# Performance work log

Measured on AMD Instinct MI355X. Metric: run time of the kernel, lower is better.

Reference implementation:

```python
import jax, jax.numpy as jnp
import numpy as np

B, S, E, NH = 1, 2048, 1024, 8
DH = E // NH
EPS_BACKEND = 1e-6  # eps in parallel_stabilized_simple
EPS_NORM = 1e-5     # MultiHeadLayerNorm (group_norm) eps


def setup_inputs() -> dict:
    key = jax.random.key(0)
    ks = jax.random.split(key, 8)
    q = jax.random.normal(ks[0], (B, S, E), jnp.float32)
    k = jax.random.normal(ks[1], (B, S, E), jnp.float32)
    v = jax.random.normal(ks[2], (B, S, E), jnp.float32)
    # gate Linear params: weight (NH, 3E), bias (NH). Small scale so gates are
    # in a realistic regime (fgate bias ~ linspace(3,6) per the torch init).
    igate_w = jax.random.normal(ks[3], (NH, 3 * E), jnp.float32) * 0.02
    igate_b = jax.random.normal(ks[4], (NH,), jnp.float32) * 0.1
    fgate_w = jax.random.normal(ks[5], (NH, 3 * E), jnp.float32) * 0.02
    fgate_b = jnp.linspace(3.0, 6.0, NH).astype(jnp.float32)
    norm_w = 1.0 + 0.1 * jax.random.normal(ks[6], (E,), jnp.float32)
    return dict(q=q, k=k, v=v, igate_w=igate_w, igate_b=igate_b,
                fgate_w=fgate_w, fgate_b=fgate_b, norm_w=norm_w)


def reference(q, k, v, igate_w, igate_b, fgate_w, fgate_b, norm_w):
    Bq, Sq, Eq = q.shape
    nh = igate_w.shape[0]
    dh = Eq // nh
    # gate pre-activations from concatenated q,k,v
    gate_in = jnp.concatenate([q, k, v], axis=-1)             # (B,S,3E)
    ig = jnp.transpose(gate_in @ igate_w.T + igate_b, (0, 2, 1))  # (B,NH,S)
    fg = jnp.transpose(gate_in @ fgate_w.T + fgate_b, (0, 2, 1))  # (B,NH,S)
    # split heads: (B,NH,S,DH)
    qh = q.reshape(Bq, Sq, nh, dh).transpose(0, 2, 1, 3)
    kh = k.reshape(Bq, Sq, nh, dh).transpose(0, 2, 1, 3)
    vh = v.reshape(Bq, Sq, nh, dh).transpose(0, 2, 1, 3)
    # cumulative log forget gates; decay matrix entry (t,s) = cs[t]-cs[s]
    log_f_cum = jnp.cumsum(jax.nn.log_sigmoid(fg), axis=-1)   # (B,NH,S)
    log_fg_mat = log_f_cum[:, :, :, None] - log_f_cum[:, :, None, :]  # (B,NH,S,S)
    ltr = jnp.tril(jnp.ones((Sq, Sq), dtype=bool))            # causal mask
    log_D = jnp.where(ltr, log_fg_mat + ig[:, :, None, :], -jnp.inf)
    # row-wise stabilizer
    max_log_D = jnp.max(log_D, axis=-1, keepdims=True)        # (B,NH,S,1)
    D = jnp.exp(log_D - max_log_D)
    qk = jnp.einsum('bhsd,bhtd->bhst', qh, kh) / jnp.sqrt(jnp.float32(dh))
    C = qk * D
    normalizer = jnp.maximum(jnp.abs(jnp.sum(C, axis=-1, keepdims=True)),
                             jnp.exp(-max_log_D))
    h = jnp.einsum('bhst,bhtd->bhsd', C / (normalizer + EPS_BACKEND), vh)
    # MultiHeadLayerNorm == group_norm with NH groups over (NH*DH), per-channel weight
    mean = jnp.mean(h, axis=-1, keepdims=True)
    var = jnp.var(h, axis=-1, keepdims=True)
    h_norm = (h - mean) / jnp.sqrt(var + EPS_NORM)
    h_norm = h_norm * norm_w.reshape(nh, dh)[None, :, None, :]
    return h_norm.transpose(0, 2, 1, 3).reshape(Bq, Sq, Eq)
```

## Files before the change

kernel.cpp:

```cpp
#include <hip/hip_runtime.h>
#include <hip/hip_bf16.h>
#include <math.h>

#define S_LEN 2048
#define E_DIM 1024
#define NHEAD 8
#define DH 128
#define E3 3072

typedef short bf16x8 __attribute__((ext_vector_type(8)));
typedef short bf16x4 __attribute__((ext_vector_type(4)));
typedef float f32x4 __attribute__((ext_vector_type(4)));
typedef float f32x16 __attribute__((ext_vector_type(16)));

#define MFMA3216(a,b,c) __builtin_amdgcn_mfma_f32_32x32x16_bf16(a,b,c,0,0,0)
#define Z16 {0.f,0.f,0.f,0.f,0.f,0.f,0.f,0.f,0.f,0.f,0.f,0.f,0.f,0.f,0.f,0.f}
#define CROW(r) (((r)&3) + 8*((r)>>2))

__device__ __forceinline__ unsigned short f2bf(float f){
  union{float f; unsigned u;} x; x.f = f;
  unsigned r = x.u + 0x7FFF + ((x.u>>16)&1);
  return (unsigned short)(r>>16);
}

__device__ __forceinline__ unsigned cvtpk(float lo, float hi){
  unsigned r;
  asm("v_cvt_pk_bf16_f32 %0, %1, %2" : "=v"(r) : "v"(lo), "v"(hi));
  return r;
}

__device__ __forceinline__ float logsigf(float x){
  return fminf(x, 0.f) - log1pf(expf(-fabsf(x)));
}

typedef const __attribute__((address_space(1))) unsigned int* gas1_t;
typedef __attribute__((address_space(3))) unsigned int* las3_t;
__device__ __forceinline__ void stage16(const ushort* g, ushort* l){
  __builtin_amdgcn_global_load_lds((gas1_t)(const void*)g, (las3_t)(void*)l, 16, 0, 0);
}

__global__ __launch_bounds__(256) void gates_qk(
    const float* __restrict__ q, const float* __restrict__ k, const float* __restrict__ v,
    const float* __restrict__ igw, const float* __restrict__ igb,
    const float* __restrict__ fgw, const float* __restrict__ fgb,
    float* __restrict__ ig_out, float* __restrict__ lsf_out,
    ushort* __restrict__ qbo, ushort* __restrict__ kbo, ushort* __restrict__ vto){
  const int t0 = blockIdx.x*4;
  const int tid = threadIdx.x;
  const int lane = tid & 63, wv = tid >> 6;
  float acc[64];
  #pragma unroll
  for (int a=0;a<64;++a) acc[a]=0.f;
  const float sc = 0.08838834764831845f;
  #pragma unroll
  for (int step=0; step<3; ++step){
    const float* src = (step==0)? q : ((step==1)? k : v);
    float4 in4[4];
    #pragma unroll
    for (int r=0;r<4;++r) in4[r] = ((const float4*)src)[(size_t)(t0+r)*256 + tid];
    if (step==0){
      #pragma unroll
      for (int r=0;r<4;++r){
        ushort4 o; o.x=f2bf(in4[r].x*sc); o.y=f2bf(in4[r].y*sc);
        o.z=f2bf(in4[r].z*sc); o.w=f2bf(in4[r].w*sc);
        ((ushort4*)qbo)[(size_t)(t0+r)*256 + tid] = o;
      }
    } else if (step==1){
      #pragma unroll
      for (int r=0;r<4;++r){
        ushort4 o; o.x=f2bf(in4[r].x); o.y=f2bf(in4[r].y);
        o.z=f2bf(in4[r].z); o.w=f2bf(in4[r].w);
        ((ushort4*)kbo)[(size_t)(t0+r)*256 + tid] = o;
      }
    } else {
      #pragma unroll
      for (int c=0;c<4;++c){
        ushort4 ov;
        ov.x = f2bf(((const float*)&in4[0])[c]);
        ov.y = f2bf(((const float*)&in4[1])[c]);
        ov.z = f2bf(((const float*)&in4[2])[c]);
        ov.w = f2bf(((const float*)&in4[3])[c]);
        *(ushort4*)(vto + (size_t)(tid*4+c)*S_LEN + t0) = ov;
      }
    }
    const int wj = step*256 + tid;
    #pragma unroll
    for (int o=0;o<8;++o){
      float4 wI = ((const float4*)igw)[o*768 + wj];
      float4 wF = ((const float4*)fgw)[o*768 + wj];
      #pragma unroll
      for (int r=0;r<4;++r){
        acc[o*4+r]    = fmaf(in4[r].x, wI.x, acc[o*4+r]);
        acc[o*4+r]    = fmaf(in4[r].y, wI.y, acc[o*4+r]);
        acc[o*4+r]    = fmaf(in4[r].z, wI.z, acc[o*4+r]);
        acc[o*4+r]    = fmaf(in4[r].w, wI.w, acc[o*4+r]);
        acc[32+o*4+r] = fmaf(in4[r].x, wF.x, acc[32+o*4+r]);
        acc[32+o*4+r] = fmaf(in4[r].y, wF.y, acc[32+o*4+r]);
        acc[32+o*4+r] = fmaf(in4[r].z, wF.z, acc[32+o*4+r]);
        acc[32+o*4+r] = fmaf(in4[r].w, wF.w, acc[32+o*4+r]);
      }
    }
  }
  int cnt = 32;
  #pragma unroll
  for (int s=0; s<6; ++s){
    const bool hib = (lane >> s) & 1;
    #pragma unroll
    for (int a=0; a<32; ++a){
      if (a < cnt){
        float sent = hib ? acc[a] : acc[a+cnt];
        float got = __shfl_xor(sent, 1<<s, 64);
        acc[a] = (hib ? acc[a+cnt] : acc[a]) + got;
      }
    }
    cnt >>= 1;
  }
  __shared__ float red[4][64];
  red[wv][lane] = acc[0];
  __syncthreads();
  if (tid < 64){
    float tot = red[0][tid]+red[1][tid]+red[2][tid]+red[3][tid];
    int a = (int)(__brev((unsigned)tid) >> 26);
    int f = a >> 5, o = (a>>2)&7, r = a&3;
    int t = t0 + r;
    if (f==0) ig_out[o*S_LEN + t] = tot + igb[o];
    else      lsf_out[o*S_LEN + t] = logsigf(tot + fgb[o]);
  }
}

__global__ __launch_bounds__(256) void scan_kernel(
    const float* __restrict__ ig, const float* __restrict__ lsf,
    float* __restrict__ cs_out, float* __restrict__ M_out, float* __restrict__ m_out){
  const int h = blockIdx.x;
  const int tid = threadIdx.x;
  __shared__ float tt[256];
  const int base = tid*8;
  const float* src = lsf + h*S_LEN;
  float loc[8]; float tot = 0.f;
  #pragma unroll
  for (int i=0;i<8;++i){ tot += src[base+i]; loc[i]=tot; }
  tt[tid]=tot; __syncthreads();
  for (int off=1; off<256; off<<=1){
    float add = (tid>=off)? tt[tid-off] : 0.f;
    __syncthreads();
    tt[tid] += add;
    __syncthreads();
  }
  const float excl = tt[tid] - tot;
  float csv[8];
  #pragma unroll
  for (int i=0;i<8;++i){ csv[i] = excl + loc[i]; cs_out[h*S_LEN+base+i]=csv[i]; }
  const float* igp = ig + h*S_LEN;
  float mloc[8], mval[8]; float mtot = -INFINITY;
  #pragma unroll
  for (int i=0;i<8;++i){
    float m = igp[base+i] - csv[i];
    mval[i] = m;
    mtot = fmaxf(mtot, m);
    mloc[i] = mtot;
  }
  __syncthreads();
  tt[tid]=mtot; __syncthreads();
  for (int off=1; off<256; off<<=1){
    float add = (tid>=off)? tt[tid-off] : -INFINITY;
    __syncthreads();
    tt[tid] = fmaxf(tt[tid], add);
    __syncthreads();
  }
  const float exclm = (tid>0)? tt[tid-1] : -INFINITY;
  #pragma unroll
  for (int i=0;i<8;++i){
    M_out[h*S_LEN+base+i] = fmaxf(exclm, mloc[i]);
    m_out[h*S_LEN+base+i] = mval[i];
  }
}

__global__ __launch_bounds__(256, 2) void mlstm_mfma6(
    const ushort* __restrict__ qb, const ushort* __restrict__ kb,
    const ushort* __restrict__ vt,
    const float* __restrict__ csb, const float* __restrict__ Mxb,
    const float* __restrict__ mbb,
    const float* __restrict__ nw, float* __restrict__ out){
  const int h = blockIdx.x;
  const int qt = 63 - blockIdx.y;
  const int tid = threadIdx.x, l = tid & 63;
  const int sq = tid >> 6;
  const int l31 = l & 31, l15 = l & 15, hi = l >> 5;

  __shared__ __align__(16) float UNI[4*32*132];
  __shared__ float MB[128];
  __shared__ float rsL[4][32];
  ushort* Kb = (ushort*)UNI;
  ushort* Vb = Kb + 16384;
  float*  Part = UNI;

  const int hS = h*S_LEN;
  const ushort* kbh = kb + h*DH;
  const ushort* vth = vt + (size_t)h*DH*S_LEN;
  const float*  mh  = mbb + hS;
  const int t0 = qt*32;
  const int NT = (t0 + 31)/128 + 1;
  const int tgq = t0 + l31;
  const float Mq = Mxb[hS + tgq];

  bf16x8 qf0,qf1,qf2,qf3,qf4,qf5,qf6,qf7;
  { const ushort* qs = qb + (size_t)tgq*E_DIM + h*DH + hi*8;
    qf0 = *(const bf16x8*)(qs+0);   qf1 = *(const bf16x8*)(qs+16);
    qf2 = *(const bf16x8*)(qs+32);  qf3 = *(const bf16x8*)(qs+48);
    qf4 = *(const bf16x8*)(qs+64);  qf5 = *(const bf16x8*)(qs+80);
    qf6 = *(const bf16x8*)(qs+96);  qf7 = *(const bf16x8*)(qs+112); }

  f32x16 a0 = Z16, a1 = Z16, a2 = Z16, a3 = Z16;
  float rsq = 0.f;

#define STAGE6(ktv) {                                                        \
    _Pragma("unroll")                                                        \
    for (int i_=0;i_<8;++i_){                                                \
      const int L_ = tid + i_*256; const int row_ = L_>>4, pc_ = L_&15;      \
      stage16(kbh + (size_t)((ktv)*128+row_)*E_DIM + ((pc_^(row_&15))<<3),   \
              Kb + (size_t)L_*8); }                                          \
    _Pragma("unroll")                                                        \
    for (int i_=0;i_<8;++i_){                                                \
      const int L_ = tid + i_*256; const int d_ = L_>>4, pc_ = L_&15;        \
      stage16(vth + (size_t)d_*S_LEN + (ktv)*128 + ((pc_^(d_&15))<<3),       \
              Vb + (size_t)L_*8); }                                          \
    if (tid < 32)                                                            \
      stage16((const ushort*)(mh + (ktv)*128) + tid*8,                       \
              (ushort*)MB + tid*8); }

#define LV6(dt, cs) (*(const bf16x8*)(Vb + (size_t)((dt)*32+l31)*128 + (((cs)^l15)<<3)))

  for (int kt=0; kt<NT; ++kt){
    if (kt) __syncthreads();
    STAGE6(kt);
    __syncthreads();

    const ushort* kbase = Kb + (size_t)(sq*32 + l31)*128;
    f32x16 cc = Z16;
    { bf16x8 ka;
      ka = *(const bf16x8*)(kbase + (((0*2+hi)^l15)<<3)); cc = MFMA3216(ka, qf0, cc);
      ka = *(const bf16x8*)(kbase + (((1*2+hi)^l15)<<3)); cc = MFMA3216(ka, qf1, cc);
      ka = *(const bf16x8*)(kbase + (((2*2+hi)^l15)<<3)); cc = MFMA3216(ka, qf2, cc);
      ka = *(const bf16x8*)(kbase + (((3*2+hi)^l15)<<3)); cc = MFMA3216(ka, qf3, cc);
      ka = *(const bf16x8*)(kbase + (((4*2+hi)^l15)<<3)); cc = MFMA3216(ka, qf4, cc);
      ka = *(const bf16x8*)(kbase + (((5*2+hi)^l15)<<3)); cc = MFMA3216(ka, qf5, cc);
      ka = *(const bf16x8*)(kbase + (((6*2+hi)^l15)<<3)); cc = MFMA3216(ka, qf6, cc);
      ka = *(const bf16x8*)(kbase + (((7*2+hi)^l15)<<3)); cc = MFMA3216(ka, qf7, cc); }

    bf16x8 fE, fO;
    {
      const int sb_ = kt*128 + sq*32 + 4*hi;
      const f32x4 mA_ = *(const f32x4*)&MB[sq*32 +  0 + 4*hi];
      const f32x4 mB_ = *(const f32x4*)&MB[sq*32 +  8 + 4*hi];
      const f32x4 mC_ = *(const f32x4*)&MB[sq*32 + 16 + 4*hi];
      const f32x4 mD_ = *(const f32x4*)&MB[sq*32 + 24 + 4*hi];
      float p0  = (sb_+0  <= tgq) ? cc[0] *__expf(mA_[0]-Mq) : 0.f;
      float p1  = (sb_+1  <= tgq) ? cc[1] *__expf(mA_[1]-Mq) : 0.f;
      float p2  = (sb_+2  <= tgq) ? cc[2] *__expf(mA_[2]-Mq) : 0.f;
      float p3  = (sb_+3  <= tgq) ? cc[3] *__expf(mA_[3]-Mq) : 0.f;
      float p4  = (sb_+8  <= tgq) ? cc[4] *__expf(mB_[0]-Mq) : 0.f;
      float p5  = (sb_+9  <= tgq) ? cc[5] *__expf(mB_[1]-Mq) : 0.f;
      float p6  = (sb_+10 <= tgq) ? cc[6] *__expf(mB_[2]-Mq) : 0.f;
      float p7  = (sb_+11 <= tgq) ? cc[7] *__expf(mB_[3]-Mq) : 0.f;
      float p8  = (sb_+16 <= tgq) ? cc[8] *__expf(mC_[0]-Mq) : 0.f;
      float p9  = (sb_+17 <= tgq) ? cc[9] *__expf(mC_[1]-Mq) : 0.f;
      float p10 = (sb_+18 <= tgq) ? cc[10]*__expf(mC_[2]-Mq) : 0.f;
      float p11 = (sb_+19 <= tgq) ? cc[11]*__expf(mC_[3]-Mq) : 0.f;
      float p12 = (sb_+24 <= tgq) ? cc[12]*__expf(mD_[0]-Mq) : 0.f;
      float p13 = (sb_+25 <= tgq) ? cc[13]*__expf(mD_[1]-Mq) : 0.f;
      float p14 = (sb_+26 <= tgq) ? cc[14]*__expf(mD_[2]-Mq) : 0.f;
      float p15 = (sb_+27 <= tgq) ? cc[15]*__expf(mD_[3]-Mq) : 0.f;
      rsq += ((p0+p1)+(p2+p3))+((p4+p5)+(p6+p7))
           + ((p8+p9)+(p10+p11))+((p12+p13)+(p14+p15));
      unsigned A0_=cvtpk(p0,p1),  A1_=cvtpk(p2,p3);
      unsigned B0_=cvtpk(p4,p5),  B1_=cvtpk(p6,p7);
      unsigned C0_=cvtpk(p8,p9),  C1_=cvtpk(p10,p11);
      unsigned D0_=cvtpk(p12,p13),D1_=cvtpk(p14,p15);
      unsigned A0x_=(unsigned)__shfl_xor((int)A0_,32,64);
      unsigned B0x_=(unsigned)__shfl_xor((int)B0_,32,64);
      unsigned A1x_=(unsigned)__shfl_xor((int)A1_,32,64);
      unsigned B1x_=(unsigned)__shfl_xor((int)B1_,32,64);
      unsigned C0x_=(unsigned)__shfl_xor((int)C0_,32,64);
      unsigned D0x_=(unsigned)__shfl_xor((int)D0_,32,64);
      unsigned C1x_=(unsigned)__shfl_xor((int)C1_,32,64);
      unsigned D1x_=(unsigned)__shfl_xor((int)D1_,32,64);
      { unsigned* u_ = (unsigned*)&fE;
        u_[0] = hi ? B0x_ : A0_;  u_[1] = hi ? B1x_ : A1_;
        u_[2] = hi ? B0_  : A0x_; u_[3] = hi ? B1_  : A1x_; }
      { unsigned* u_ = (unsigned*)&fO;
        u_[0] = hi ? D0x_ : C0_;  u_[1] = hi ? D1x_ : C1_;
        u_[2] = hi ? D0_  : C0x_; u_[3] = hi ? D1_  : C1x_; }
    }

    a0 = MFMA3216(fE, LV6(0, sq*4 + 0 + hi), a0);
    a1 = MFMA3216(fE, LV6(1, sq*4 + 0 + hi), a1);
    a2 = MFMA3216(fE, LV6(2, sq*4 + 0 + hi), a2);
    a3 = MFMA3216(fE, LV6(3, sq*4 + 0 + hi), a3);
    a0 = MFMA3216(fO, LV6(0, sq*4 + 2 + hi), a0);
    a1 = MFMA3216(fO, LV6(1, sq*4 + 2 + hi), a1);
    a2 = MFMA3216(fO, LV6(2, sq*4 + 2 + hi), a2);
    a3 = MFMA3216(fO, LV6(3, sq*4 + 2 + hi), a3);
  }

  __syncthreads();
  #pragma unroll
  for (int r=0;r<16;++r){
    const int qrow = CROW(r) + 4*hi;
    float* pr = Part + (size_t)(sq*32 + qrow)*132 + l31;
    pr[0]  = a0[r];
    pr[32] = a1[r];
    pr[64] = a2[r];
    pr[96] = a3[r];
  }
  rsq += __shfl_xor(rsq, 32, 64);
  if (l < 32) rsL[sq][l31] = rsq;
  __syncthreads();

  {
    const int q = tid >> 3, dg = tid & 7;
    f32x4 os0={0.f,0.f,0.f,0.f}, os1=os0, os2=os0, os3=os0;
    #pragma unroll
    for (int w2=0; w2<4; ++w2){
      const float* pb = Part + (size_t)(w2*32 + q)*132 + dg*16;
      os0 += *(const f32x4*)(pb+0);
      os1 += *(const f32x4*)(pb+4);
      os2 += *(const f32x4*)(pb+8);
      os3 += *(const f32x4*)(pb+12);
    }
    const float rstot = rsL[0][q]+rsL[1][q]+rsL[2][q]+rsL[3][q];
    const int tq = t0 + q;
    const float en = __expf(-(csb[hS+tq] + Mxb[hS+tq]));
    const float iv = 1.f/(fmaxf(fabsf(rstot), en) + 1e-6f);
    f32x4 h0, h1, h2, h3;
    h0[0]=os0[0]*iv; h0[1]=os0[1]*iv; h0[2]=os0[2]*iv; h0[3]=os0[3]*iv;
    h1[0]=os1[0]*iv; h1[1]=os1[1]*iv; h1[2]=os1[2]*iv; h1[3]=os1[3]*iv;
    h2[0]=os2[0]*iv; h2[1]=os2[1]*iv; h2[2]=os2[2]*iv; h2[3]=os2[3]*iv;
    h3[0]=os3[0]*iv; h3[1]=os3[1]*iv; h3[2]=os3[2]*iv; h3[3]=os3[3]*iv;
    float s1 = (h0[0]+h0[1]+h0[2]+h0[3]) + (h1[0]+h1[1]+h1[2]+h1[3])
             + (h2[0]+h2[1]+h2[2]+h2[3]) + (h3[0]+h3[1]+h3[2]+h3[3]);
    float s2 = (h0[0]*h0[0]+h0[1]*h0[1]+h0[2]*h0[2]+h0[3]*h0[3])
             + (h1[0]*h1[0]+h1[1]*h1[1]+h1[2]*h1[2]+h1[3]*h1[3])
             + (h2[0]*h2[0]+h2[1]*h2[1]+h2[2]*h2[2]+h2[3]*h2[3])
             + (h3[0]*h3[0]+h3[1]*h3[1]+h3[2]*h3[2]+h3[3]*h3[3]);
    s1 += __shfl_xor(s1, 1, 64);  s2 += __shfl_xor(s2, 1, 64);
    s1 += __shfl_xor(s1, 2, 64);  s2 += __shfl_xor(s2, 2, 64);
    s1 += __shfl_xor(s1, 4, 64);  s2 += __shfl_xor(s2, 4, 64);
    const float mean = s1*(1.f/128.f);
    const float var  = s2*(1.f/128.f) - mean*mean;
    const float rstd = rsqrtf(var + 1e-5f);
    const float* nb = nw + h*DH + dg*16;
    const f32x4 n0 = *(const f32x4*)(nb+0);
    const f32x4 n1 = *(const f32x4*)(nb+4);
    const f32x4 n2 = *(const f32x4*)(nb+8);
    const f32x4 n3 = *(const f32x4*)(nb+12);
    float* ob = out + (size_t)tq*E_DIM + h*DH + dg*16;
    f32x4 o0v, o1v, o2v, o3v;
    o0v[0]=(h0[0]-mean)*rstd*n0[0]; o0v[1]=(h0[1]-mean)*rstd*n0[1];
    o0v[2]=(h0[2]-mean)*rstd*n0[2]; o0v[3]=(h0[3]-mean)*rstd*n0[3];
    o1v[0]=(h1[0]-mean)*rstd*n1[0]; o1v[1]=(h1[1]-mean)*rstd*n1[1];
    o1v[2]=(h1[2]-mean)*rstd*n1[2]; o1v[3]=(h1[3]-mean)*rstd*n1[3];
    o2v[0]=(h2[0]-mean)*rstd*n2[0]; o2v[1]=(h2[1]-mean)*rstd*n2[1];
    o2v[2]=(h2[2]-mean)*rstd*n2[2]; o2v[3]=(h2[3]-mean)*rstd*n2[3];
    o3v[0]=(h3[0]-mean)*rstd*n3[0]; o3v[1]=(h3[1]-mean)*rstd*n3[1];
    o3v[2]=(h3[2]-mean)*rstd*n3[2]; o3v[3]=(h3[3]-mean)*rstd*n3[3];
    *(f32x4*)(ob+0)  = o0v;
    *(f32x4*)(ob+4)  = o1v;
    *(f32x4*)(ob+8)  = o2v;
    *(f32x4*)(ob+12) = o3v;
  }
}

extern "C" void kernel_launch(void* const* d_in, const int* in_sizes, int n_in,
                              void* d_out, int out_size, void* d_ws, size_t ws_size,
                              hipStream_t stream) {
  const float* q   = (const float*)d_in[0];
  const float* k   = (const float*)d_in[1];
  const float* v   = (const float*)d_in[2];
  const float* igw = (const float*)d_in[3];
  const float* igb = (const float*)d_in[4];
  const float* fgw = (const float*)d_in[5];
  const float* fgb = (const float*)d_in[6];
  const float* nw  = (const float*)d_in[7];
  float* outp = (float*)d_out;

  float* ws  = (float*)d_ws;
  float* ig  = ws;
  float* lsf = ws + 1*NHEAD*S_LEN;
  float* csb = ws + 2*NHEAD*S_LEN;
  float* Mb  = ws + 3*NHEAD*S_LEN;
  float* mbf = ws + 4*NHEAD*S_LEN;
  ushort* qbb = (ushort*)(ws + 5*NHEAD*S_LEN);
  ushort* kbb = qbb + (size_t)S_LEN*E_DIM;
  ushort* vtb = kbb + (size_t)S_LEN*E_DIM;

  gates_qk<<<S_LEN/4, 256, 0, stream>>>(q, k, v, igw, igb, fgw, fgb,
                                        ig, lsf, qbb, kbb, vtb);
  scan_kernel<<<NHEAD, 256, 0, stream>>>(ig, lsf, csb, Mb, mbf);
  mlstm_mfma6<<<dim3(NHEAD, 64), 256, 0, stream>>>(qbb, kbb, vtb, csb, Mb, mbf, nw, outp);
}
```

Baseline: 61.39 us.

## Double-buffer K/V tiles and process 64 queries per 512-thread block

```diff
diff --git a/kernel.cpp b/kernel.cpp
--- a/kernel.cpp
+++ b/kernel.cpp
@@ -175,32 +175,32 @@
   }
 }
 
-__global__ __launch_bounds__(256, 2) void mlstm_mfma6(
+__global__ __launch_bounds__(512, 2) void mlstm_mfma8(
     const ushort* __restrict__ qb, const ushort* __restrict__ kb,
     const ushort* __restrict__ vt,
     const float* __restrict__ csb, const float* __restrict__ Mxb,
     const float* __restrict__ mbb,
     const float* __restrict__ nw, float* __restrict__ out){
   const int h = blockIdx.x;
-  const int qt = 63 - blockIdx.y;
+  const int qt = 31 - blockIdx.y;
   const int tid = threadIdx.x, l = tid & 63;
-  const int sq = tid >> 6;
+  const int w = tid >> 6;
+  const int sq = w & 3, qh = w >> 2;
   const int l31 = l & 31, l15 = l & 15, hi = l >> 5;
 
-  __shared__ __align__(16) float UNI[4*32*132];
-  __shared__ float MB[128];
+  __shared__ __align__(16) float UNI[32768];
+  __shared__ float MB[2][128];
   __shared__ float rsL[4][32];
-  ushort* Kb = (ushort*)UNI;
-  ushort* Vb = Kb + 16384;
-  float*  Part = UNI;
+  ushort* KV = (ushort*)UNI;
+  float* Part = UNI;
 
   const int hS = h*S_LEN;
   const ushort* kbh = kb + h*DH;
   const ushort* vth = vt + (size_t)h*DH*S_LEN;
   const float*  mh  = mbb + hS;
-  const int t0 = qt*32;
-  const int NT = (t0 + 31)/128 + 1;
-  const int tgq = t0 + l31;
+  const int t0 = qt*64;
+  const int NT = (t0 + 63)/128 + 1;
+  const int tgq = t0 + qh*32 + l31;
   const float Mq = Mxb[hS + tgq];
 
   bf16x8 qf0,qf1,qf2,qf3,qf4,qf5,qf6,qf7;
@@ -213,29 +213,34 @@
   f32x16 a0 = Z16, a1 = Z16, a2 = Z16, a3 = Z16;
   float rsq = 0.f;
 
-#define STAGE6(ktv) {                                                        \
+#define STAGE8(ktv, bb) {                                                    \
+    ushort* kd_ = KV + (bb)*32768;                                           \
+    ushort* vd_ = kd_ + 16384;                                               \
     _Pragma("unroll")                                                        \
-    for (int i_=0;i_<8;++i_){                                                \
-      const int L_ = tid + i_*256; const int row_ = L_>>4, pc_ = L_&15;      \
+    for (int i_=0;i_<4;++i_){                                                \
+      const int L_ = tid + i_*512; const int row_ = L_>>4, pc_ = L_&15;      \
       stage16(kbh + (size_t)((ktv)*128+row_)*E_DIM + ((pc_^(row_&15))<<3),   \
-              Kb + (size_t)L_*8); }                                          \
+              kd_ + (size_t)L_*8); }                                         \
     _Pragma("unroll")                                                        \
-    for (int i_=0;i_<8;++i_){                                                \
-      const int L_ = tid + i_*256; const int d_ = L_>>4, pc_ = L_&15;        \
+    for (int i_=0;i_<4;++i_){                                                \
+      const int L_ = tid + i_*512; const int d_ = L_>>4, pc_ = L_&15;        \
       stage16(vth + (size_t)d_*S_LEN + (ktv)*128 + ((pc_^(d_&15))<<3),       \
-              Vb + (size_t)L_*8); }                                          \
+              vd_ + (size_t)L_*8); }                                         \
     if (tid < 32)                                                            \
       stage16((const ushort*)(mh + (ktv)*128) + tid*8,                       \
-              (ushort*)MB + tid*8); }
-
-#define LV6(dt, cs) (*(const bf16x8*)(Vb + (size_t)((dt)*32+l31)*128 + (((cs)^l15)<<3)))
-
+              (ushort*)&MB[bb][0] + tid*8); }
+
+  STAGE8(0, 0);
+  int buf = 0;
   for (int kt=0; kt<NT; ++kt){
-    if (kt) __syncthreads();
-    STAGE6(kt);
-    __syncthreads();
-
-    const ushort* kbase = Kb + (size_t)(sq*32 + l31)*128;
+    __syncthreads();
+    if (kt+1 < NT){ STAGE8(kt+1, buf^1); }
+
+    const ushort* Kc = KV + buf*32768;
+    const ushort* Vc = Kc + 16384;
+    const float*  Mc = &MB[buf][0];
+
+    const ushort* kbase = Kc + (size_t)(sq*32 + l31)*128;
     f32x16 cc = Z16;
     { bf16x8 ka;
       ka = *(const bf16x8*)(kbase + (((0*2+hi)^l15)<<3)); cc = MFMA3216(ka, qf0, cc);
@@ -250,10 +255,10 @@
     bf16x8 fE, fO;
     {
       const int sb_ = kt*128 + sq*32 + 4*hi;
-      const f32x4 mA_ = *(const f32x4*)&MB[sq*32 +  0 + 4*hi];
-      const f32x4 mB_ = *(const f32x4*)&MB[sq*32 +  8 + 4*hi];
-      const f32x4 mC_ = *(const f32x4*)&MB[sq*32 + 16 + 4*hi];
-      const f32x4 mD_ = *(const f32x4*)&MB[sq*32 + 24 + 4*hi];
+      const f32x4 mA_ = *(const f32x4*)&Mc[sq*32 +  0 + 4*hi];
+      const f32x4 mB_ = *(const f32x4*)&Mc[sq*32 +  8 + 4*hi];
+      const f32x4 mC_ = *(const f32x4*)&Mc[sq*32 + 16 + 4*hi];
+      const f32x4 mD_ = *(const f32x4*)&Mc[sq*32 + 24 + 4*hi];
       float p0  = (sb_+0  <= tgq) ? cc[0] *__expf(mA_[0]-Mq) : 0.f;
       float p1  = (sb_+1  <= tgq) ? cc[1] *__expf(mA_[1]-Mq) : 0.f;
       float p2  = (sb_+2  <= tgq) ? cc[2] *__expf(mA_[2]-Mq) : 0.f;
@@ -292,81 +297,75 @@
         u_[2] = hi ? D0_  : C0x_; u_[3] = hi ? D1_  : C1x_; }
     }
 
-    a0 = MFMA3216(fE, LV6(0, sq*4 + 0 + hi), a0);
-    a1 = MFMA3216(fE, LV6(1, sq*4 + 0 + hi), a1);
-    a2 = MFMA3216(fE, LV6(2, sq*4 + 0 + hi), a2);
-    a3 = MFMA3216(fE, LV6(3, sq*4 + 0 + hi), a3);
-    a0 = MFMA3216(fO, LV6(0, sq*4 + 2 + hi), a0);
-    a1 = MFMA3216(fO, LV6(1, sq*4 + 2 + hi), a1);
-    a2 = MFMA3216(fO, LV6(2, sq*4 + 2 + hi), a2);
-    a3 = MFMA3216(fO, LV6(3, sq*4 + 2 + hi), a3);
-  }
-
-  __syncthreads();
-  #pragma unroll
-  for (int r=0;r<16;++r){
-    const int qrow = CROW(r) + 4*hi;
-    float* pr = Part + (size_t)(sq*32 + qrow)*132 + l31;
-    pr[0]  = a0[r];
-    pr[32] = a1[r];
-    pr[64] = a2[r];
-    pr[96] = a3[r];
-  }
-  rsq += __shfl_xor(rsq, 32, 64);
-  if (l < 32) rsL[sq][l31] = rsq;
-  __syncthreads();
-
-  {
-    const int q = tid >> 3, dg = tid & 7;
-    f32x4 os0={0.f,0.f,0.f,0.f}, os1=os0, os2=os0, os3=os0;
-    #pragma unroll
-    for (int w2=0; w2<4; ++w2){
-      const float* pb = Part + (size_t)(w2*32 + q)*132 + dg*16;
-      os0 += *(const f32x4*)(pb+0);
-      os1 += *(const f32x4*)(pb+4);
-      os2 += *(const f32x4*)(pb+8);
-      os3 += *(const f32x4*)(pb+12);
-    }
-    const float rstot = rsL[0][q]+rsL[1][q]+rsL[2][q]+rsL[3][q];
-    const int tq = t0 + q;
-    const float en = __expf(-(csb[hS+tq] + Mxb[hS+tq]));
-    const float iv = 1.f/(fmaxf(fabsf(rstot), en) + 1e-6f);
-    f32x4 h0, h1, h2, h3;
-    h0[0]=os0[0]*iv; h0[1]=os0[1]*iv; h0[2]=os0[2]*iv; h0[3]=os0[3]*iv;
-    h1[0]=os1[0]*iv; h1[1]=os1[1]*iv; h1[2]=os1[2]*iv; h1[3]=os1[3]*iv;
-    h2[0]=os2[0]*iv; h2[1]=os2[1]*iv; h2[2]=os2[2]*iv; h2[3]=os2[3]*iv;
-    h3[0]=os3[0]*iv; h3[1]=os3[1]*iv; h3[2]=os3[2]*iv; h3[3]=os3[3]*iv;
-    float s1 = (h0[0]+h0[1]+h0[2]+h0[3]) + (h1[0]+h1[1]+h1[2]+h1[3])
-             + (h2[0]+h2[1]+h2[2]+h2[3]) + (h3[0]+h3[1]+h3[2]+h3[3]);
-    float s2 = (h0[0]*h0[0]+h0[1]*h0[1]+h0[2]*h0[2]+h0[3]*h0[3])
-             + (h1[0]*h1[0]+h1[1]*h1[1]+h1[2]*h1[2]+h1[3]*h1[3])
-             + (h2[0]*h2[0]+h2[1]*h2[1]+h2[2]*h2[2]+h2[3]*h2[3])
-             + (h3[0]*h3[0]+h3[1]*h3[1]+h3[2]*h3[2]+h3[3]*h3[3]);
-    s1 += __shfl_xor(s1, 1, 64);  s2 += __shfl_xor(s2, 1, 64);
-    s1 += __shfl_xor(s1, 2, 64);  s2 += __shfl_xor(s2, 2, 64);
-    s1 += __shfl_xor(s1, 4, 64);  s2 += __shfl_xor(s2, 4, 64);
-    const float mean = s1*(1.f/128.f);
-    const float var  = s2*(1.f/128.f) - mean*mean;
-    const float rstd = rsqrtf(var + 1e-5f);
-    const float* nb = nw + h*DH + dg*16;
-    const f32x4 n0 = *(const f32x4*)(nb+0);
-    const f32x4 n1 = *(const f32x4*)(nb+4);
-    const f32x4 n2 = *(const f32x4*)(nb+8);
-    const f32x4 n3 = *(const f32x4*)(nb+12);
-    float* ob = out + (size_t)tq*E_DIM + h*DH + dg*16;
-    f32x4 o0v, o1v, o2v, o3v;
-    o0v[0]=(h0[0]-mean)*rstd*n0[0]; o0v[1]=(h0[1]-mean)*rstd*n0[1];
-    o0v[2]=(h0[2]-mean)*rstd*n0[2]; o0v[3]=(h0[3]-mean)*rstd*n0[3];
-    o1v[0]=(h1[0]-mean)*rstd*n1[0]; o1v[1]=(h1[1]-mean)*rstd*n1[1];
-    o1v[2]=(h1[2]-mean)*rstd*n1[2]; o1v[3]=(h1[3]-mean)*rstd*n1[3];
-    o2v[0]=(h2[0]-mean)*rstd*n2[0]; o2v[1]=(h2[1]-mean)*rstd*n2[1];
-    o2v[2]=(h2[2]-mean)*rstd*n2[2]; o2v[3]=(h2[3]-mean)*rstd*n2[3];
-    o3v[0]=(h3[0]-mean)*rstd*n3[0]; o3v[1]=(h3[1]-mean)*rstd*n3[1];
-    o3v[2]=(h3[2]-mean)*rstd*n3[2]; o3v[3]=(h3[3]-mean)*rstd*n3[3];
-    *(f32x4*)(ob+0)  = o0v;
-    *(f32x4*)(ob+4)  = o1v;
-    *(f32x4*)(ob+8)  = o2v;
-    *(f32x4*)(ob+12) = o3v;
+#define LV8(dt, cs) (*(const bf16x8*)(Vc + (size_t)((dt)*32+l31)*128 + (((cs)^l15)<<3)))
+    a0 = MFMA3216(fE, LV8(0, sq*4 + 0 + hi), a0);
+    a1 = MFMA3216(fE, LV8(1, sq*4 + 0 + hi), a1);
+    a2 = MFMA3216(fE, LV8(2, sq*4 + 0 + hi), a2);
+    a3 = MFMA3216(fE, LV8(3, sq*4 + 0 + hi), a3);
+    a0 = MFMA3216(fO, LV8(0, sq*4 + 2 + hi), a0);
+    a1 = MFMA3216(fO, LV8(1, sq*4 + 2 + hi), a1);
+    a2 = MFMA3216(fO, LV8(2, sq*4 + 2 + hi), a2);
+    a3 = MFMA3216(fO, LV8(3, sq*4 + 2 + hi), a3);
+#undef LV8
+    buf ^= 1;
+  }
+
+  #pragma unroll
+  for (int r2=0; r2<2; ++r2){
+    __syncthreads();
+    if (qh == r2){
+      #pragma unroll
+      for (int r=0;r<16;++r){
+        const int qrow = CROW(r) + 4*hi;
+        float* pr = Part + (size_t)(sq*32 + qrow)*132 + l31;
+        pr[0]  = a0[r];
+        pr[32] = a1[r];
+        pr[64] = a2[r];
+        pr[96] = a3[r];
+      }
+      float rs2 = rsq + __shfl_xor(rsq, 32, 64);
+      if (l < 32) rsL[sq][l31] = rs2;
+    }
+    __syncthreads();
+    {
+      const int q = tid >> 4;
+      const int dg = tid & 15;
+      f32x4 osA={0.f,0.f,0.f,0.f}, osB=osA;
+      #pragma unroll
+      for (int w2=0; w2<4; ++w2){
+        const float* pb = Part + (size_t)(w2*32 + q)*132 + dg*8;
+        osA += *(const f32x4*)(pb+0);
+        osB += *(const f32x4*)(pb+4);
+      }
+      const float rstot = rsL[0][q]+rsL[1][q]+rsL[2][q]+rsL[3][q];
+      const int tq = t0 + r2*32 + q;
+      const float en = __expf(-(csb[hS+tq] + Mxb[hS+tq]));
+      const float iv = 1.f/(fmaxf(fabsf(rstot), en) + 1e-6f);
+      f32x4 hA, hB;
+      hA[0]=osA[0]*iv; hA[1]=osA[1]*iv; hA[2]=osA[2]*iv; hA[3]=osA[3]*iv;
+      hB[0]=osB[0]*iv; hB[1]=osB[1]*iv; hB[2]=osB[2]*iv; hB[3]=osB[3]*iv;
+      float s1 = (hA[0]+hA[1]+hA[2]+hA[3]) + (hB[0]+hB[1]+hB[2]+hB[3]);
+      float s2 = (hA[0]*hA[0]+hA[1]*hA[1]+hA[2]*hA[2]+hA[3]*hA[3])
+               + (hB[0]*hB[0]+hB[1]*hB[1]+hB[2]*hB[2]+hB[3]*hB[3]);
+      s1 += __shfl_xor(s1, 1, 64);  s2 += __shfl_xor(s2, 1, 64);
+      s1 += __shfl_xor(s1, 2, 64);  s2 += __shfl_xor(s2, 2, 64);
+      s1 += __shfl_xor(s1, 4, 64);  s2 += __shfl_xor(s2, 4, 64);
+      s1 += __shfl_xor(s1, 8, 64);  s2 += __shfl_xor(s2, 8, 64);
+      const float mean = s1*(1.f/128.f);
+      const float var  = s2*(1.f/128.f) - mean*mean;
+      const float rstd = rsqrtf(var + 1e-5f);
+      const float* nb = nw + h*DH + dg*8;
+      const f32x4 n0 = *(const f32x4*)(nb+0);
+      const f32x4 n1 = *(const f32x4*)(nb+4);
+      float* ob = out + (size_t)tq*E_DIM + h*DH + dg*8;
+      f32x4 oA, oB;
+      oA[0]=(hA[0]-mean)*rstd*n0[0]; oA[1]=(hA[1]-mean)*rstd*n0[1];
+      oA[2]=(hA[2]-mean)*rstd*n0[2]; oA[3]=(hA[3]-mean)*rstd*n0[3];
+      oB[0]=(hB[0]-mean)*rstd*n1[0]; oB[1]=(hB[1]-mean)*rstd*n1[1];
+      oB[2]=(hB[2]-mean)*rstd*n1[2]; oB[3]=(hB[3]-mean)*rstd*n1[3];
+      *(f32x4*)(ob+0) = oA;
+      *(f32x4*)(ob+4) = oB;
+    }
   }
 }
 
@@ -396,5 +395,5 @@
   gates_qk<<<S_LEN/4, 256, 0, stream>>>(q, k, v, igw, igb, fgw, fgb,
                                         ig, lsf, qbb, kbb, vtb);
   scan_kernel<<<NHEAD, 256, 0, stream>>>(ig, lsf, csb, Mb, mbf);
-  mlstm_mfma6<<<dim3(NHEAD, 64), 256, 0, stream>>>(qbb, kbb, vtb, csb, Mb, mbf, nw, outp);
-}
+  mlstm_mfma8<<<dim3(NHEAD, 32), 512, 0, stream>>>(qbb, kbb, vtb, csb, Mb, mbf, nw, outp);
+}
```

Measured after the change: 64.70 us. 1.05x slower.

## Load K tiles directly into registers with double-buffered prefetch

Applied to the files above, without the earlier changes.

```diff
diff --git a/kernel.cpp b/kernel.cpp
--- a/kernel.cpp
+++ b/kernel.cpp
@@ -175,7 +175,89 @@
   }
 }
 
-__global__ __launch_bounds__(256, 2) void mlstm_mfma6(
+#define LOADK9(ktv, S) {                                                     \
+    const ushort* kr_ = kbh + (size_t)((ktv)*128 + sq*32 + l31)*E_DIM + hi*8; \
+    ck##S##0 = *(const bf16x8*)(kr_+0);   ck##S##1 = *(const bf16x8*)(kr_+16);\
+    ck##S##2 = *(const bf16x8*)(kr_+32);  ck##S##3 = *(const bf16x8*)(kr_+48);\
+    ck##S##4 = *(const bf16x8*)(kr_+64);  ck##S##5 = *(const bf16x8*)(kr_+80);\
+    ck##S##6 = *(const bf16x8*)(kr_+96);  ck##S##7 = *(const bf16x8*)(kr_+112); }
+
+#define STAGE_V9(ktv) {                                                      \
+    _Pragma("unroll")                                                        \
+    for (int i_=0;i_<8;++i_){                                                \
+      const int L_ = tid + i_*256; const int d_ = L_>>4, pc_ = L_&15;        \
+      stage16(vth + (size_t)d_*S_LEN + (ktv)*128 + ((pc_^(d_&15))<<3),       \
+              Vb + (size_t)L_*8); }                                          \
+    if (tid < 32)                                                            \
+      stage16((const ushort*)(mh + (ktv)*128) + tid*8,                       \
+              (ushort*)MB + tid*8); }
+
+#define LV9(dt, cs) (*(const bf16x8*)(Vb + (size_t)((dt)*32+l31)*128 + (((cs)^l15)<<3)))
+
+#define COMPUTE9(S) {                                                        \
+    f32x16 cc = Z16;                                                         \
+    cc = MFMA3216(ck##S##0, qf0, cc);                                        \
+    cc = MFMA3216(ck##S##1, qf1, cc);                                        \
+    cc = MFMA3216(ck##S##2, qf2, cc);                                        \
+    cc = MFMA3216(ck##S##3, qf3, cc);                                        \
+    cc = MFMA3216(ck##S##4, qf4, cc);                                        \
+    cc = MFMA3216(ck##S##5, qf5, cc);                                        \
+    cc = MFMA3216(ck##S##6, qf6, cc);                                        \
+    cc = MFMA3216(ck##S##7, qf7, cc);                                        \
+    bf16x8 fE, fO;                                                           \
+    {                                                                        \
+      const int sb_ = kt*128 + sq*32 + 4*hi;                                 \
+      const f32x4 mA_ = *(const f32x4*)&MB[sq*32 +  0 + 4*hi];               \
+      const f32x4 mB_ = *(const f32x4*)&MB[sq*32 +  8 + 4*hi];               \
+      const f32x4 mC_ = *(const f32x4*)&MB[sq*32 + 16 + 4*hi];               \
+      const f32x4 mD_ = *(const f32x4*)&MB[sq*32 + 24 + 4*hi];               \
+      float p0  = (sb_+0  <= tgq) ? cc[0] *__expf(mA_[0]-Mq) : 0.f;          \
+      float p1  = (sb_+1  <= tgq) ? cc[1] *__expf(mA_[1]-Mq) : 0.f;          \
+      float p2  = (sb_+2  <= tgq) ? cc[2] *__expf(mA_[2]-Mq) : 0.f;          \
+      float p3  = (sb_+3  <= tgq) ? cc[3] *__expf(mA_[3]-Mq) : 0.f;          \
+      float p4  = (sb_+8  <= tgq) ? cc[4] *__expf(mB_[0]-Mq) : 0.f;          \
+      float p5  = (sb_+9  <= tgq) ? cc[5] *__expf(mB_[1]-Mq) : 0.f;          \
+      float p6  = (sb_+10 <= tgq) ? cc[6] *__expf(mB_[2]-Mq) : 0.f;          \
+      float p7  = (sb_+11 <= tgq) ? cc[7] *__expf(mB_[3]-Mq) : 0.f;          \
+      float p8  = (sb_+16 <= tgq) ? cc[8] *__expf(mC_[0]-Mq) : 0.f;          \
+      float p9  = (sb_+17 <= tgq) ? cc[9] *__expf(mC_[1]-Mq) : 0.f;          \
+      float p10 = (sb_+18 <= tgq) ? cc[10]*__expf(mC_[2]-Mq) : 0.f;          \
+      float p11 = (sb_+19 <= tgq) ? cc[11]*__expf(mC_[3]-Mq) : 0.f;          \
+      float p12 = (sb_+24 <= tgq) ? cc[12]*__expf(mD_[0]-Mq) : 0.f;          \
+      float p13 = (sb_+25 <= tgq) ? cc[13]*__expf(mD_[1]-Mq) : 0.f;          \
+      float p14 = (sb_+26 <= tgq) ? cc[14]*__expf(mD_[2]-Mq) : 0.f;          \
+      float p15 = (sb_+27 <= tgq) ? cc[15]*__expf(mD_[3]-Mq) : 0.f;          \
+      rsq += ((p0+p1)+(p2+p3))+((p4+p5)+(p6+p7))                             \
+           + ((p8+p9)+(p10+p11))+((p12+p13)+(p14+p15));                      \
+      unsigned A0_=cvtpk(p0,p1),  A1_=cvtpk(p2,p3);                          \
+      unsigned B0_=cvtpk(p4,p5),  B1_=cvtpk(p6,p7);                          \
+      unsigned C0_=cvtpk(p8,p9),  C1_=cvtpk(p10,p11);                        \
+      unsigned D0_=cvtpk(p12,p13),D1_=cvtpk(p14,p15);                        \
+      unsigned A0x_=(unsigned)__shfl_xor((int)A0_,32,64);                    \
+      unsigned B0x_=(unsigned)__shfl_xor((int)B0_,32,64);                    \
+      unsigned A1x_=(unsigned)__shfl_xor((int)A1_,32,64);                    \
+      unsigned B1x_=(unsigned)__shfl_xor((int)B1_,32,64);                    \
+      unsigned C0x_=(unsigned)__shfl_xor((int)C0_,32,64);                    \
+      unsigned D0x_=(unsigned)__shfl_xor((int)D0_,32,64);                    \
+      unsigned C1x_=(unsigned)__shfl_xor((int)C1_,32,64);                    \
+      unsigned D1x_=(unsigned)__shfl_xor((int)D1_,32,64);                    \
+      { unsigned* u_ = (unsigned*)&fE;                                       \
+        u_[0] = hi ? B0x_ : A0_;  u_[1] = hi ? B1x_ : A1_;                   \
+        u_[2] = hi ? B0_  : A0x_; u_[3] = hi ? B1_  : A1x_; }                \
+      { unsigned* u_ = (unsigned*)&fO;                                       \
+        u_[0] = hi ? D0x_ : C0_;  u_[1] = hi ? D1x_ : C1_;                   \
+        u_[2] = hi ? D0_  : C0x_; u_[3] = hi ? D1_  : C1x_; }                \
+    }                                                                        \
+    a0 = MFMA3216(fE, LV9(0, sq*4 + 0 + hi), a0);                            \
+    a1 = MFMA3216(fE, LV9(1, sq*4 + 0 + hi), a1);                            \
+    a2 = MFMA3216(fE, LV9(2, sq*4 + 0 + hi), a2);                            \
+    a3 = MFMA3216(fE, LV9(3, sq*4 + 0 + hi), a3);                            \
+    a0 = MFMA3216(fO, LV9(0, sq*4 + 2 + hi), a0);                            \
+    a1 = MFMA3216(fO, LV9(1, sq*4 + 2 + hi), a1);                            \
+    a2 = MFMA3216(fO, LV9(2, sq*4 + 2 + hi), a2);                            \
+    a3 = MFMA3216(fO, LV9(3, sq*4 + 2 + hi), a3); }
+
+__global__ __launch_bounds__(256, 2) void mlstm_mfma9(
     const ushort* __restrict__ qb, const ushort* __restrict__ kb,
     const ushort* __restrict__ vt,
     const float* __restrict__ csb, const float* __restrict__ Mxb,
@@ -190,8 +272,7 @@
   __shared__ __align__(16) float UNI[4*32*132];
   __shared__ float MB[128];
   __shared__ float rsL[4][32];
-  ushort* Kb = (ushort*)UNI;
-  ushort* Vb = Kb + 16384;
+  ushort* Vb = (ushort*)UNI;
   float*  Part = UNI;
 
   const int hS = h*S_LEN;
@@ -213,93 +294,25 @@
   f32x16 a0 = Z16, a1 = Z16, a2 = Z16, a3 = Z16;
   float rsq = 0.f;
 
-#define STAGE6(ktv) {                                                        \
-    _Pragma("unroll")                                                        \
-    for (int i_=0;i_<8;++i_){                                                \
-      const int L_ = tid + i_*256; const int row_ = L_>>4, pc_ = L_&15;      \
-      stage16(kbh + (size_t)((ktv)*128+row_)*E_DIM + ((pc_^(row_&15))<<3),   \
-              Kb + (size_t)L_*8); }                                          \
-    _Pragma("unroll")                                                        \
-    for (int i_=0;i_<8;++i_){                                                \
-      const int L_ = tid + i_*256; const int d_ = L_>>4, pc_ = L_&15;        \
-      stage16(vth + (size_t)d_*S_LEN + (ktv)*128 + ((pc_^(d_&15))<<3),       \
-              Vb + (size_t)L_*8); }                                          \
-    if (tid < 32)                                                            \
-      stage16((const ushort*)(mh + (ktv)*128) + tid*8,                       \
-              (ushort*)MB + tid*8); }
-
-#define LV6(dt, cs) (*(const bf16x8*)(Vb + (size_t)((dt)*32+l31)*128 + (((cs)^l15)<<3)))
-
-  for (int kt=0; kt<NT; ++kt){
+  bf16x8 ckA0,ckA1,ckA2,ckA3,ckA4,ckA5,ckA6,ckA7;
+  bf16x8 ckB0,ckB1,ckB2,ckB3,ckB4,ckB5,ckB6,ckB7;
+
+  LOADK9(0, A);
+  int kt = 0;
+  while (true){
     if (kt) __syncthreads();
-    STAGE6(kt);
-    __syncthreads();
-
-    const ushort* kbase = Kb + (size_t)(sq*32 + l31)*128;
-    f32x16 cc = Z16;
-    { bf16x8 ka;
-      ka = *(const bf16x8*)(kbase + (((0*2+hi)^l15)<<3)); cc = MFMA3216(ka, qf0, cc);
-      ka = *(const bf16x8*)(kbase + (((1*2+hi)^l15)<<3)); cc = MFMA3216(ka, qf1, cc);
-      ka = *(const bf16x8*)(kbase + (((2*2+hi)^l15)<<3)); cc = MFMA3216(ka, qf2, cc);
-      ka = *(const bf16x8*)(kbase + (((3*2+hi)^l15)<<3)); cc = MFMA3216(ka, qf3, cc);
-      ka = *(const bf16x8*)(kbase + (((4*2+hi)^l15)<<3)); cc = MFMA3216(ka, qf4, cc);
-      ka = *(const bf16x8*)(kbase + (((5*2+hi)^l15)<<3)); cc = MFMA3216(ka, qf5, cc);
-      ka = *(const bf16x8*)(kbase + (((6*2+hi)^l15)<<3)); cc = MFMA3216(ka, qf6, cc);
-      ka = *(const bf16x8*)(kbase + (((7*2+hi)^l15)<<3)); cc = MFMA3216(ka, qf7, cc); }
-
-    bf16x8 fE, fO;
-    {
-      const int sb_ = kt*128 + sq*32 + 4*hi;
-      const f32x4 mA_ = *(const f32x4*)&MB[sq*32 +  0 + 4*hi];
-      const f32x4 mB_ = *(const f32x4*)&MB[sq*32 +  8 + 4*hi];
-      const f32x4 mC_ = *(const f32x4*)&MB[sq*32 + 16 + 4*hi];
-      const f32x4 mD_ = *(const f32x4*)&MB[sq*32 + 24 + 4*hi];
-      float p0  = (sb_+0  <= tgq) ? cc[0] *__expf(mA_[0]-Mq) : 0.f;
-      float p1  = (sb_+1  <= tgq) ? cc[1] *__expf(mA_[1]-Mq) : 0.f;
-      float p2  = (sb_+2  <= tgq) ? cc[2] *__expf(mA_[2]-Mq) : 0.f;
-      float p3  = (sb_+3  <= tgq) ? cc[3] *__expf(mA_[3]-Mq) : 0.f;
-      float p4  = (sb_+8  <= tgq) ? cc[4] *__expf(mB_[0]-Mq) : 0.f;
-      float p5  = (sb_+9  <= tgq) ? cc[5] *__expf(mB_[1]-Mq) : 0.f;
-      float p6  = (sb_+10 <= tgq) ? cc[6] *__expf(mB_[2]-Mq) : 0.f;
-      float p7  = (sb_+11 <= tgq) ? cc[7] *__expf(mB_[3]-Mq) : 0.f;
-      float p8  = (sb_+16 <= tgq) ? cc[8] *__expf(mC_[0]-Mq) : 0.f;
-      float p9  = (sb_+17 <= tgq) ? cc[9] *__expf(mC_[1]-Mq) : 0.f;
-      float p10 = (sb_+18 <= tgq) ? cc[10]*__expf(mC_[2]-Mq) : 0.f;
-      float p11 = (sb_+19 <= tgq) ? cc[11]*__expf(mC_[3]-Mq) : 0.f;
-      float p12 = (sb_+24 <= tgq) ? cc[12]*__expf(mD_[0]-Mq) : 0.f;
-      float p13 = (sb_+25 <= tgq) ? cc[13]*__expf(mD_[1]-Mq) : 0.f;
-      float p14 = (sb_+26 <= tgq) ? cc[14]*__expf(mD_[2]-Mq) : 0.f;
-      float p15 = (sb_+27 <= tgq) ? cc[15]*__expf(mD_[3]-Mq) : 0.f;
-      rsq += ((p0+p1)+(p2+p3))+((p4+p5)+(p6+p7))
-           + ((p8+p9)+(p10+p11))+((p12+p13)+(p14+p15));
-      unsigned A0_=cvtpk(p0,p1),  A1_=cvtpk(p2,p3);
-      unsigned B0_=cvtpk(p4,p5),  B1_=cvtpk(p6,p7);
-      unsigned C0_=cvtpk(p8,p9),  C1_=cvtpk(p10,p11);
-      unsigned D0_=cvtpk(p12,p13),D1_=cvtpk(p14,p15);
-      unsigned A0x_=(unsigned)__shfl_xor((int)A0_,32,64);
-      unsigned B0x_=(unsigned)__shfl_xor((int)B0_,32,64);
-      unsigned A1x_=(unsigned)__shfl_xor((int)A1_,32,64);
-      unsigned B1x_=(unsigned)__shfl_xor((int)B1_,32,64);
-      unsigned C0x_=(unsigned)__shfl_xor((int)C0_,32,64);
-      unsigned D0x_=(unsigned)__shfl_xor((int)D0_,32,64);
-      unsigned C1x_=(unsigned)__shfl_xor((int)C1_,32,64);
-      unsigned D1x_=(unsigned)__shfl_xor((int)D1_,32,64);
-      { unsigned* u_ = (unsigned*)&fE;
-        u_[0] = hi ? B0x_ : A0_;  u_[1] = hi ? B1x_ : A1_;
-        u_[2] = hi ? B0_  : A0x_; u_[3] = hi ? B1_  : A1x_; }
-      { unsigned* u_ = (unsigned*)&fO;
-        u_[0] = hi ? D0x_ : C0_;  u_[1] = hi ? D1x_ : C1_;
-        u_[2] = hi ? D0_  : C0x_; u_[3] = hi ? D1_  : C1x_; }
-    }
-
-    a0 = MFMA3216(fE, LV6(0, sq*4 + 0 + hi), a0);
-    a1 = MFMA3216(fE, LV6(1, sq*4 + 0 + hi), a1);
-    a2 = MFMA3216(fE, LV6(2, sq*4 + 0 + hi), a2);
-    a3 = MFMA3216(fE, LV6(3, sq*4 + 0 + hi), a3);
-    a0 = MFMA3216(fO, LV6(0, sq*4 + 2 + hi), a0);
-    a1 = MFMA3216(fO, LV6(1, sq*4 + 2 + hi), a1);
-    a2 = MFMA3216(fO, LV6(2, sq*4 + 2 + hi), a2);
-    a3 = MFMA3216(fO, LV6(3, sq*4 + 2 + hi), a3);
+    STAGE_V9(kt);
+    if (kt+1 < NT) LOADK9(kt+1, B);
+    __syncthreads();
+    COMPUTE9(A);
+    ++kt; if (kt == NT) break;
+
+    __syncthreads();
+    STAGE_V9(kt);
+    if (kt+1 < NT) LOADK9(kt+1, A);
+    __syncthreads();
+    COMPUTE9(B);
+    ++kt; if (kt == NT) break;
   }
 
   __syncthreads();
@@ -396,5 +409,5 @@
   gates_qk<<<S_LEN/4, 256, 0, stream>>>(q, k, v, igw, igb, fgw, fgb,
                                         ig, lsf, qbb, kbb, vtb);
   scan_kernel<<<NHEAD, 256, 0, stream>>>(ig, lsf, csb, Mb, mbf);
-  mlstm_mfma6<<<dim3(NHEAD, 64), 256, 0, stream>>>(qbb, kbb, vtb, csb, Mb, mbf, nw, outp);
-}
+  mlstm_mfma9<<<dim3(NHEAD, 64), 256, 0, stream>>>(qbb, kbb, vtb, csb, Mb, mbf, nw, outp);
+}
```

Result: slower. 95.82 us (+56.1%).
